# Performance work log

Hardware: AMD Instinct MI355X
Metric: run time of the kernel (lower is better)

The kernel has to match this reference:

```python
import jax, jax.numpy as jnp
import numpy as np

N_NODES = 50000
N_EDGES = 600000
N_GRAPHS = 256
IN_C = 128
HID = 128
OUT_C = 2


def setup_inputs() -> dict:
    key = jax.random.key(0)
    ks = jax.random.split(key, 16)
    d = {}
    d["x"] = jax.random.normal(ks[0], (N_NODES, IN_C), jnp.float32)
    d["edge_index"] = jax.random.randint(ks[1], (2, N_EDGES), 0, N_NODES, dtype=jnp.int32)
    d["root_node_idx"] = jax.random.randint(ks[2], (N_GRAPHS,), 0, N_NODES, dtype=jnp.int32)
    d["batch"] = jnp.sort(jax.random.randint(ks[3], (N_NODES,), 0, N_GRAPHS, dtype=jnp.int32))
    dims = [(IN_C, HID), (HID, HID), (HID, HID), (HID, HID)]
    for i, (ci, co) in enumerate(dims, start=1):
        s = 1.0 / np.sqrt(ci)
        d[f"w{i}_l"] = jax.random.uniform(ks[3 + i], (co, ci), jnp.float32, -s, s)
        d[f"b{i}_l"] = jnp.zeros((co,), jnp.float32)
        d[f"w{i}_r"] = jax.random.uniform(ks[7 + i], (co, ci), jnp.float32, -s, s)
    s = 1.0 / np.sqrt(2 * HID)
    d["w_cls"] = jax.random.uniform(ks[12], (OUT_C, 2 * HID), jnp.float32, -s, s)
    d["b_cls"] = jnp.zeros((OUT_C,), jnp.float32)
    return d


def _sage_conv(x, src, tgt, deg_inv, w_l, b_l, w_r):
    # mean aggregation of source features at target nodes (PyG SAGEConv, aggr='mean')
    agg = jax.ops.segment_sum(x[src], tgt, num_segments=N_NODES) * deg_inv  # [N, C]
    # out = lin_l(agg) + lin_r(x); lin_r has no bias in PyG SAGEConv
    return agg @ w_l.T + b_l + x @ w_r.T


def reference(x, edge_index, root_node_idx, batch,
              w1_l, b1_l, w1_r, w2_l, b2_l, w2_r,
              w3_l, b3_l, w3_r, w4_l, b4_l, w4_r,
              w_cls, b_cls):
    src, tgt = edge_index[0], edge_index[1]
    ones_e = jnp.ones((src.shape[0],), x.dtype)
    deg = jax.ops.segment_sum(ones_e, tgt, num_segments=N_NODES)
    deg_inv = (1.0 / jnp.maximum(deg, 1.0))[:, None]  # [N, 1]

    h = jax.nn.relu(_sage_conv(x, src, tgt, deg_inv, w1_l, b1_l, w1_r))
    h = jax.nn.relu(_sage_conv(h, src, tgt, deg_inv, w2_l, b2_l, w2_r))
    h = jax.nn.relu(_sage_conv(h, src, tgt, deg_inv, w3_l, b3_l, w3_r))
    h = jax.nn.relu(_sage_conv(h, src, tgt, deg_inv, w4_l, b4_l, w4_r))

    root_emb = h[root_node_idx]  # [G, HID]
    g_sum = jax.ops.segment_sum(h, batch, num_segments=N_GRAPHS)
    g_cnt = jax.ops.segment_sum(jnp.ones((h.shape[0],), h.dtype), batch, num_segments=N_GRAPHS)
    graph_emb = g_sum / jnp.maximum(g_cnt, 1.0)[:, None]  # [G, HID]

    combined = jnp.concatenate([root_emb, graph_emb], axis=1)  # [G, 2*HID]
    return combined @ w_cls.T + b_cls  # [G, OUT_C]
```

## Files before the change

kernel.cpp:

```cpp
#include <hip/hip_runtime.h>
#include <hip/hip_bf16.h>

#define N_NODES 50000
#define N_EDGES 600000
#define N_GRAPHS 256
#define C 128
#define NB 196

typedef unsigned short ushort;
typedef unsigned int uint;
typedef __attribute__((ext_vector_type(8))) short bfrag8;
typedef __attribute__((ext_vector_type(4))) float facc4;

__device__ __forceinline__ ushort f2bf(float v) {
    uint u = __float_as_uint(v);
    u += 0x7FFFu + ((u >> 16) & 1u);
    return (ushort)(u >> 16);
}
__device__ __forceinline__ float bf2f(ushort u) {
    return __uint_as_float(((uint)u) << 16);
}
__device__ __forceinline__ void fsplit(float v, ushort& h, ushort& l) {
    h = f2bf(v);
    l = f2bf(v - bf2f(h));
}

__global__ void k_deg(const int* __restrict__ tgt, int* __restrict__ deg) {
    int e = blockIdx.x * blockDim.x + threadIdx.x;
    if (e < N_EDGES) atomicAdd(&deg[tgt[e]], 1);
}

__global__ __launch_bounds__(256) void k_bsum(const int* __restrict__ deg,
                                              int* __restrict__ bsum,
                                              float* __restrict__ dinv) {
    __shared__ int ws[4];
    int idx = blockIdx.x * 256 + threadIdx.x;
    int v = (idx < N_NODES) ? deg[idx] : 0;
    if (idx < N_NODES) dinv[idx] = 1.0f / fmaxf((float)v, 1.0f);
    int s = v;
#pragma unroll
    for (int off = 1; off < 64; off <<= 1) s += __shfl_xor(s, off);
    if ((threadIdx.x & 63) == 0) ws[threadIdx.x >> 6] = s;
    __syncthreads();
    if (threadIdx.x == 0) bsum[blockIdx.x] = ws[0] + ws[1] + ws[2] + ws[3];
}

__global__ __launch_bounds__(256) void k_bscan(const int* __restrict__ bsum,
                                               int* __restrict__ boff,
                                               int* __restrict__ rowptr) {
    __shared__ int ws[4];
    int t = threadIdx.x, lane = t & 63, w = t >> 6;
    int v = (t < NB) ? bsum[t] : 0;
    int incl = v;
#pragma unroll
    for (int off = 1; off < 64; off <<= 1) {
        int u = __shfl_up(incl, off);
        if (lane >= off) incl += u;
    }
    if (lane == 63) ws[w] = incl;
    __syncthreads();
    int wo = 0;
    if (w > 0) wo += ws[0];
    if (w > 1) wo += ws[1];
    if (w > 2) wo += ws[2];
    if (t < NB) boff[t] = wo + incl - v;
    if (t == 0) rowptr[N_NODES] = N_EDGES;
}

__global__ __launch_bounds__(256) void k_rowptr(const int* __restrict__ deg,
                                                const int* __restrict__ boff,
                                                int* __restrict__ rowptr) {
    __shared__ int ws[4];
    int b = blockIdx.x, t = threadIdx.x;
    int idx = b * 256 + t;
    int lane = t & 63, w = t >> 6;
    int v = (idx < N_NODES) ? deg[idx] : 0;
    int incl = v;
#pragma unroll
    for (int off = 1; off < 64; off <<= 1) {
        int u = __shfl_up(incl, off);
        if (lane >= off) incl += u;
    }
    if (lane == 63) ws[w] = incl;
    __syncthreads();
    int wo = 0;
    if (w > 0) wo += ws[0];
    if (w > 1) wo += ws[1];
    if (w > 2) wo += ws[2];
    if (idx < N_NODES) rowptr[idx] = boff[b] + wo + incl - v;
}

__global__ void k_fill(const int* __restrict__ src, const int* __restrict__ tgt,
                       const int* __restrict__ rowptr, int* __restrict__ fill,
                       int* __restrict__ csr_src) {
    int e = blockIdx.x * blockDim.x + threadIdx.x;
    if (e >= N_EDGES) return;
    int d = tgt[e];
    int pos = atomicAdd(&fill[d], 1);
    csr_src[rowptr[d] + pos] = src[e];
}

__global__ __launch_bounds__(256) void k_xsplit(const float* __restrict__ x,
                                                ushort* __restrict__ Ahi,
                                                ushort* __restrict__ Alo) {
    int gid = blockIdx.x * 256 + threadIdx.x;
    if (gid >= N_NODES * 32) return;
    int n = gid >> 5, c4 = (gid & 31) << 2;
    float4 v = *(const float4*)(x + (size_t)n * C + c4);
    ushort4 h, l;
    fsplit(v.x, h.x, l.x); fsplit(v.y, h.y, l.y);
    fsplit(v.z, h.z, l.z); fsplit(v.w, h.w, l.w);
    *(ushort4*)(Ahi + (size_t)n * 256 + 128 + c4) = h;
    *(ushort4*)(Alo + (size_t)n * 256 + 128 + c4) = l;
}

struct WPtrs { const float* wl[4]; const float* wr[4]; };
__global__ __launch_bounds__(256) void k_wsplit(WPtrs wp, ushort* __restrict__ BTh,
                                                ushort* __restrict__ BTl) {
    int gid = blockIdx.x * 256 + threadIdx.x;
    if (gid >= 4 * 128 * 256) return;
    int l = gid >> 15;
    int rem = gid & 32767;
    int n = rem >> 8, k = rem & 255;
    float v = (k < 128) ? wp.wl[l][n * 128 + k] : wp.wr[l][n * 128 + (k - 128)];
    ushort h, lo;
    fsplit(v, h, lo);
    BTh[gid] = h;
    BTl[gid] = lo;
}

__global__ __launch_bounds__(256) void k_gather(const ushort* __restrict__ Ahi_r,
                                                const ushort* __restrict__ Alo_r,
                                                ushort* __restrict__ Ahi_w,
                                                ushort* __restrict__ Alo_w,
                                                const int* __restrict__ csr_src,
                                                const int* __restrict__ rowptr,
                                                const float* __restrict__ dinv) {
    int node = blockIdx.x * 8 + (threadIdx.x >> 5);
    if (node >= N_NODES) return;
    int lane = threadIdx.x & 31;
    int c4 = lane << 2;
    int s = rowptr[node], e = rowptr[node + 1];
    float a0 = 0.f, a1 = 0.f, a2 = 0.f, a3 = 0.f;
    int j = s;
    for (; j + 1 < e; j += 2) {
        int s0 = csr_src[j], s1 = csr_src[j + 1];
        ushort4 h0 = *(const ushort4*)(Ahi_r + (size_t)s0 * 256 + 128 + c4);
        ushort4 l0 = *(const ushort4*)(Alo_r + (size_t)s0 * 256 + 128 + c4);
        ushort4 h1 = *(const ushort4*)(Ahi_r + (size_t)s1 * 256 + 128 + c4);
        ushort4 l1 = *(const ushort4*)(Alo_r + (size_t)s1 * 256 + 128 + c4);
        a0 += bf2f(h0.x) + bf2f(l0.x) + bf2f(h1.x) + bf2f(l1.x);
        a1 += bf2f(h0.y) + bf2f(l0.y) + bf2f(h1.y) + bf2f(l1.y);
        a2 += bf2f(h0.z) + bf2f(l0.z) + bf2f(h1.z) + bf2f(l1.z);
        a3 += bf2f(h0.w) + bf2f(l0.w) + bf2f(h1.w) + bf2f(l1.w);
    }
    if (j < e) {
        int s0 = csr_src[j];
        ushort4 h0 = *(const ushort4*)(Ahi_r + (size_t)s0 * 256 + 128 + c4);
        ushort4 l0 = *(const ushort4*)(Alo_r + (size_t)s0 * 256 + 128 + c4);
        a0 += bf2f(h0.x) + bf2f(l0.x);
        a1 += bf2f(h0.y) + bf2f(l0.y);
        a2 += bf2f(h0.z) + bf2f(l0.z);
        a3 += bf2f(h0.w) + bf2f(l0.w);
    }
    float sc = dinv[node];
    a0 *= sc; a1 *= sc; a2 *= sc; a3 *= sc;
    ushort4 h, l;
    fsplit(a0, h.x, l.x); fsplit(a1, h.y, l.y);
    fsplit(a2, h.z, l.z); fsplit(a3, h.w, l.w);
    *(ushort4*)(Ahi_w + (size_t)node * 256 + c4) = h;
    *(ushort4*)(Alo_w + (size_t)node * 256 + c4) = l;
}

__global__ __launch_bounds__(256, 2) void k_gemm(const ushort* __restrict__ Ahi,
                                                 const ushort* __restrict__ Alo,
                                                 const ushort* __restrict__ BTh,
                                                 const ushort* __restrict__ BTl,
                                                 const float* __restrict__ bl,
                                                 ushort* __restrict__ Hhi,
                                                 ushort* __restrict__ Hlo) {
    __shared__ short As[2][128][40];
    __shared__ short Bs[2][128][40];
    const int tid = threadIdx.x;
    const int wave = tid >> 6, lane = tid & 63;
    const int m0 = blockIdx.x * 128;
    const int wm = (wave & 1) * 64;
    const int wn = (wave >> 1) * 64;
    const int l15 = lane & 15, lk = (lane >> 4) * 8;

    facc4 acc[4][4] = {};

    for (int k0 = 0; k0 < 256; k0 += 32) {
        __syncthreads();
#pragma unroll
        for (int i = 0; i < 2; i++) {
            int idx = tid * 2 + i;
            int r = idx >> 2, seg = (idx & 3) * 8;
            int gr = m0 + r; gr = gr < N_NODES ? gr : N_NODES - 1;
            bfrag8 vh = *(const bfrag8*)(Ahi + (size_t)gr * 256 + k0 + seg);
            bfrag8 vl = *(const bfrag8*)(Alo + (size_t)gr * 256 + k0 + seg);
            *(bfrag8*)&As[0][r][seg] = vh;
            *(bfrag8*)&As[1][r][seg] = vl;
            bfrag8 bh = *(const bfrag8*)(BTh + r * 256 + k0 + seg);
            bfrag8 bo = *(const bfrag8*)(BTl + r * 256 + k0 + seg);
            *(bfrag8*)&Bs[0][r][seg] = bh;
            *(bfrag8*)&Bs[1][r][seg] = bo;
        }
        __syncthreads();
        bfrag8 a[2][4], b[2][4];
#pragma unroll
        for (int t = 0; t < 4; t++) {
            a[0][t] = *(const bfrag8*)&As[0][wm + t * 16 + l15][lk];
            a[1][t] = *(const bfrag8*)&As[1][wm + t * 16 + l15][lk];
            b[0][t] = *(const bfrag8*)&Bs[0][wn + t * 16 + l15][lk];
            b[1][t] = *(const bfrag8*)&Bs[1][wn + t * 16 + l15][lk];
        }
#pragma unroll
        for (int mt = 0; mt < 4; mt++)
#pragma unroll
            for (int nt = 0; nt < 4; nt++) {
                acc[mt][nt] = __builtin_amdgcn_mfma_f32_16x16x32_bf16(a[0][mt], b[0][nt], acc[mt][nt], 0, 0, 0);
                acc[mt][nt] = __builtin_amdgcn_mfma_f32_16x16x32_bf16(a[0][mt], b[1][nt], acc[mt][nt], 0, 0, 0);
                acc[mt][nt] = __builtin_amdgcn_mfma_f32_16x16x32_bf16(a[1][mt], b[0][nt], acc[mt][nt], 0, 0, 0);
            }
    }
    const int r4 = (lane >> 4) * 4;
#pragma unroll
    for (int mt = 0; mt < 4; mt++) {
#pragma unroll
        for (int nt = 0; nt < 4; nt++) {
            int col = wn + nt * 16 + l15;
            float bias = bl[col];
#pragma unroll
            for (int r = 0; r < 4; r++) {
                int grow = m0 + wm + mt * 16 + r4 + r;
                if (grow < N_NODES) {
                    float v = fmaxf(acc[mt][nt][r] + bias, 0.f);
                    ushort h, l;
                    fsplit(v, h, l);
                    Hhi[(size_t)grow * 256 + 128 + col] = h;
                    Hlo[(size_t)grow * 256 + 128 + col] = l;
                }
            }
        }
    }
}

__global__ void k_gstart(const int* __restrict__ batch, int* __restrict__ gstart) {
    int g = blockIdx.x * blockDim.x + threadIdx.x;
    if (g > N_GRAPHS) return;
    int lo = 0, hi = N_NODES;
    while (lo < hi) {
        int mid = (lo + hi) >> 1;
        if (batch[mid] < g) lo = mid + 1;
        else hi = mid;
    }
    gstart[g] = lo;
}

__global__ __launch_bounds__(512) void k_pool(const ushort* __restrict__ Ahi,
                                              const ushort* __restrict__ Alo,
                                              const int* __restrict__ gstart,
                                              float* __restrict__ gmean) {
    __shared__ float part[4][C];
    int g = blockIdx.x;
    int c = threadIdx.x & 127, p = threadIdx.x >> 7;
    int s = gstart[g], e = gstart[g + 1];
    float sum = 0.f;
    for (int n = s + p; n < e; n += 4) {
        size_t o = (size_t)n * 256 + 128 + c;
        sum += bf2f(Ahi[o]) + bf2f(Alo[o]);
    }
    part[p][c] = sum;
    __syncthreads();
    if (p == 0) {
        float tot = part[0][c] + part[1][c] + part[2][c] + part[3][c];
        float cnt = fmaxf((float)(e - s), 1.0f);
        gmean[g * C + c] = tot / cnt;
    }
}

__global__ __launch_bounds__(256) void k_final(const ushort* __restrict__ Ahi,
                                               const ushort* __restrict__ Alo,
                                               const float* __restrict__ gmean,
                                               const int* __restrict__ root,
                                               const float* __restrict__ wcls,
                                               const float* __restrict__ bcls,
                                               float* __restrict__ out) {
    __shared__ float red[8];
    int g = blockIdx.x, t = threadIdx.x;
    float v;
    if (t < 128) {
        size_t o = (size_t)root[g] * 256 + 128 + t;
        v = bf2f(Ahi[o]) + bf2f(Alo[o]);
    } else {
        v = gmean[g * C + (t - 128)];
    }
    float p0 = v * wcls[t];
    float p1 = v * wcls[256 + t];
#pragma unroll
    for (int off = 32; off; off >>= 1) {
        p0 += __shfl_down(p0, off);
        p1 += __shfl_down(p1, off);
    }
    int wid = t >> 6;
    if ((t & 63) == 0) { red[wid] = p0; red[4 + wid] = p1; }
    __syncthreads();
    if (t == 0) {
        out[g * 2 + 0] = red[0] + red[1] + red[2] + red[3] + bcls[0];
        out[g * 2 + 1] = red[4] + red[5] + red[6] + red[7] + bcls[1];
    }
}

extern "C" void kernel_launch(void* const* d_in, const int* in_sizes, int n_in,
                              void* d_out, int out_size, void* d_ws, size_t ws_size,
                              hipStream_t stream) {
    const float* x = (const float*)d_in[0];
    const int* ei = (const int*)d_in[1];
    const int* src = ei;
    const int* tgt = ei + N_EDGES;
    const int* root = (const int*)d_in[2];
    const int* batch = (const int*)d_in[3];
    WPtrs wp;
    wp.wl[0] = (const float*)d_in[4];  wp.wr[0] = (const float*)d_in[6];
    wp.wl[1] = (const float*)d_in[7];  wp.wr[1] = (const float*)d_in[9];
    wp.wl[2] = (const float*)d_in[10]; wp.wr[2] = (const float*)d_in[12];
    wp.wl[3] = (const float*)d_in[13]; wp.wr[3] = (const float*)d_in[15];
    const float* blv[4] = {(const float*)d_in[5], (const float*)d_in[8],
                           (const float*)d_in[11], (const float*)d_in[14]};
    const float* wcls = (const float*)d_in[16];
    const float* bcls = (const float*)d_in[17];
    float* out = (float*)d_out;

    ushort* Ahi = (ushort*)d_ws;
    ushort* Alo = Ahi + (size_t)N_NODES * 256;
    ushort* BTh = Alo + (size_t)N_NODES * 256;
    ushort* BTl = BTh + 4 * 128 * 256;
    int* deg = (int*)(BTl + 4 * 128 * 256);
    float* dinv = (float*)(deg + N_NODES);
    int* rowptr = (int*)(dinv + N_NODES);
    int* fill = rowptr + N_NODES + 1;
    int* csr_src = fill + N_NODES;
    int* bsum = csr_src + N_EDGES;
    int* boff = bsum + 256;
    int* gstart = boff + 256;
    float* gmean = (float*)(gstart + 260);

    hipMemsetAsync(deg, 0, N_NODES * sizeof(int), stream);
    hipMemsetAsync(fill, 0, N_NODES * sizeof(int), stream);
    k_deg<<<(N_EDGES + 255) / 256, 256, 0, stream>>>(tgt, deg);
    k_bsum<<<NB, 256, 0, stream>>>(deg, bsum, dinv);
    k_bscan<<<1, 256, 0, stream>>>(bsum, boff, rowptr);
    k_rowptr<<<NB, 256, 0, stream>>>(deg, boff, rowptr);
    k_fill<<<(N_EDGES + 255) / 256, 256, 0, stream>>>(src, tgt, rowptr, fill, csr_src);
    k_gstart<<<1, 512, 0, stream>>>(batch, gstart);
    k_xsplit<<<(N_NODES * 32 + 255) / 256, 256, 0, stream>>>(x, Ahi, Alo);
    k_wsplit<<<(4 * 128 * 256 + 255) / 256, 256, 0, stream>>>(wp, BTh, BTl);

    for (int l = 0; l < 4; l++) {
        k_gather<<<(N_NODES + 7) / 8, 256, 0, stream>>>(Ahi, Alo, Ahi, Alo,
                                                        csr_src, rowptr, dinv);
        k_gemm<<<(N_NODES + 127) / 128, 256, 0, stream>>>(
            Ahi, Alo, BTh + l * 32768, BTl + l * 32768, blv[l], Ahi, Alo);
    }
    k_pool<<<N_GRAPHS, 512, 0, stream>>>(Ahi, Alo, gstart, gmean);
    k_final<<<N_GRAPHS, 256, 0, stream>>>(Ahi, Alo, gmean, root, wcls, bcls, out);
}
```

Measured before the change: 501.1 us.

## Prefetch next K-tile into registers in GEMM and unroll gather loop by four

Measured after the change: 486.4 us. 1.03x faster.

```diff
diff --git a/kernel.cpp b/kernel.cpp
--- a/kernel.cpp
+++ b/kernel.cpp
@@ -143,18 +143,27 @@
     int s = rowptr[node], e = rowptr[node + 1];
     float a0 = 0.f, a1 = 0.f, a2 = 0.f, a3 = 0.f;
     int j = s;
-    for (; j + 1 < e; j += 2) {
+    for (; j + 3 < e; j += 4) {
         int s0 = csr_src[j], s1 = csr_src[j + 1];
+        int s2 = csr_src[j + 2], s3 = csr_src[j + 3];
         ushort4 h0 = *(const ushort4*)(Ahi_r + (size_t)s0 * 256 + 128 + c4);
         ushort4 l0 = *(const ushort4*)(Alo_r + (size_t)s0 * 256 + 128 + c4);
         ushort4 h1 = *(const ushort4*)(Ahi_r + (size_t)s1 * 256 + 128 + c4);
         ushort4 l1 = *(const ushort4*)(Alo_r + (size_t)s1 * 256 + 128 + c4);
-        a0 += bf2f(h0.x) + bf2f(l0.x) + bf2f(h1.x) + bf2f(l1.x);
-        a1 += bf2f(h0.y) + bf2f(l0.y) + bf2f(h1.y) + bf2f(l1.y);
-        a2 += bf2f(h0.z) + bf2f(l0.z) + bf2f(h1.z) + bf2f(l1.z);
-        a3 += bf2f(h0.w) + bf2f(l0.w) + bf2f(h1.w) + bf2f(l1.w);
-    }
-    if (j < e) {
+        ushort4 h2 = *(const ushort4*)(Ahi_r + (size_t)s2 * 256 + 128 + c4);
+        ushort4 l2 = *(const ushort4*)(Alo_r + (size_t)s2 * 256 + 128 + c4);
+        ushort4 h3 = *(const ushort4*)(Ahi_r + (size_t)s3 * 256 + 128 + c4);
+        ushort4 l3 = *(const ushort4*)(Alo_r + (size_t)s3 * 256 + 128 + c4);
+        a0 += (bf2f(h0.x) + bf2f(l0.x)) + (bf2f(h1.x) + bf2f(l1.x))
+            + (bf2f(h2.x) + bf2f(l2.x)) + (bf2f(h3.x) + bf2f(l3.x));
+        a1 += (bf2f(h0.y) + bf2f(l0.y)) + (bf2f(h1.y) + bf2f(l1.y))
+            + (bf2f(h2.y) + bf2f(l2.y)) + (bf2f(h3.y) + bf2f(l3.y));
+        a2 += (bf2f(h0.z) + bf2f(l0.z)) + (bf2f(h1.z) + bf2f(l1.z))
+            + (bf2f(h2.z) + bf2f(l2.z)) + (bf2f(h3.z) + bf2f(l3.z));
+        a3 += (bf2f(h0.w) + bf2f(l0.w)) + (bf2f(h1.w) + bf2f(l1.w))
+            + (bf2f(h2.w) + bf2f(l2.w)) + (bf2f(h3.w) + bf2f(l3.w));
+    }
+    for (; j < e; j++) {
         int s0 = csr_src[j];
         ushort4 h0 = *(const ushort4*)(Ahi_r + (size_t)s0 * 256 + 128 + c4);
         ushort4 l0 = *(const ushort4*)(Alo_r + (size_t)s0 * 256 + 128 + c4);
@@ -172,13 +181,13 @@
     *(ushort4*)(Alo_w + (size_t)node * 256 + c4) = l;
 }
 
-__global__ __launch_bounds__(256, 2) void k_gemm(const ushort* __restrict__ Ahi,
-                                                 const ushort* __restrict__ Alo,
-                                                 const ushort* __restrict__ BTh,
-                                                 const ushort* __restrict__ BTl,
-                                                 const float* __restrict__ bl,
-                                                 ushort* __restrict__ Hhi,
-                                                 ushort* __restrict__ Hlo) {
+__global__ __launch_bounds__(256) void k_gemm(const ushort* __restrict__ Ahi,
+                                              const ushort* __restrict__ Alo,
+                                              const ushort* __restrict__ BTh,
+                                              const ushort* __restrict__ BTl,
+                                              const float* __restrict__ bl,
+                                              ushort* __restrict__ Hhi,
+                                              ushort* __restrict__ Hlo) {
     __shared__ short As[2][128][40];
     __shared__ short Bs[2][128][40];
     const int tid = threadIdx.x;
@@ -188,25 +197,32 @@
     const int wn = (wave >> 1) * 64;
     const int l15 = lane & 15, lk = (lane >> 4) * 8;
 
+    const int sr = tid >> 1;
+    const int sc = (tid & 1) * 16;
+    int garow = m0 + sr; if (garow >= N_NODES) garow = N_NODES - 1;
+    const ushort* pAh = Ahi + (size_t)garow * 256 + sc;
+    const ushort* pAl = Alo + (size_t)garow * 256 + sc;
+    const ushort* pBh = BTh + sr * 256 + sc;
+    const ushort* pBl = BTl + sr * 256 + sc;
+
+    bfrag8 rAh0, rAh1, rAl0, rAl1, rBh0, rBh1, rBl0, rBl1;
+#define LOADSTEP(K0) do { \
+        rAh0 = *(const bfrag8*)(pAh + (K0));     rAh1 = *(const bfrag8*)(pAh + (K0) + 8); \
+        rAl0 = *(const bfrag8*)(pAl + (K0));     rAl1 = *(const bfrag8*)(pAl + (K0) + 8); \
+        rBh0 = *(const bfrag8*)(pBh + (K0));     rBh1 = *(const bfrag8*)(pBh + (K0) + 8); \
+        rBl0 = *(const bfrag8*)(pBl + (K0));     rBl1 = *(const bfrag8*)(pBl + (K0) + 8); \
+    } while (0)
+
+    LOADSTEP(0);
     facc4 acc[4][4] = {};
-
-    for (int k0 = 0; k0 < 256; k0 += 32) {
+#pragma unroll
+    for (int s = 0; s < 8; s++) {
+        *(bfrag8*)&As[0][sr][sc]     = rAh0;  *(bfrag8*)&As[0][sr][sc + 8] = rAh1;
+        *(bfrag8*)&As[1][sr][sc]     = rAl0;  *(bfrag8*)&As[1][sr][sc + 8] = rAl1;
+        *(bfrag8*)&Bs[0][sr][sc]     = rBh0;  *(bfrag8*)&Bs[0][sr][sc + 8] = rBh1;
+        *(bfrag8*)&Bs[1][sr][sc]     = rBl0;  *(bfrag8*)&Bs[1][sr][sc + 8] = rBl1;
         __syncthreads();
-#pragma unroll
-        for (int i = 0; i < 2; i++) {
-            int idx = tid * 2 + i;
-            int r = idx >> 2, seg = (idx & 3) * 8;
-            int gr = m0 + r; gr = gr < N_NODES ? gr : N_NODES - 1;
-            bfrag8 vh = *(const bfrag8*)(Ahi + (size_t)gr * 256 + k0 + seg);
-            bfrag8 vl = *(const bfrag8*)(Alo + (size_t)gr * 256 + k0 + seg);
-            *(bfrag8*)&As[0][r][seg] = vh;
-            *(bfrag8*)&As[1][r][seg] = vl;
-            bfrag8 bh = *(const bfrag8*)(BTh + r * 256 + k0 + seg);
-            bfrag8 bo = *(const bfrag8*)(BTl + r * 256 + k0 + seg);
-            *(bfrag8*)&Bs[0][r][seg] = bh;
-            *(bfrag8*)&Bs[1][r][seg] = bo;
-        }
-        __syncthreads();
+        if (s < 7) LOADSTEP((s + 1) * 32);
         bfrag8 a[2][4], b[2][4];
 #pragma unroll
         for (int t = 0; t < 4; t++) {
@@ -223,7 +239,10 @@
                 acc[mt][nt] = __builtin_amdgcn_mfma_f32_16x16x32_bf16(a[0][mt], b[1][nt], acc[mt][nt], 0, 0, 0);
                 acc[mt][nt] = __builtin_amdgcn_mfma_f32_16x16x32_bf16(a[1][mt], b[0][nt], acc[mt][nt], 0, 0, 0);
             }
-    }
+        __syncthreads();
+    }
+#undef LOADSTEP
+
     const int r4 = (lane >> 4) * 4;
 #pragma unroll
     for (int mt = 0; mt < 4; mt++) {
```
